# Optimization experiments

Hardware: AMD Instinct MI355X
Metric: run time of the kernel (lower is better)

Reference implementation:

```python
import jax, jax.numpy as jnp
import numpy as np

DIM0, DIMO, WIDTH, DEPTH = 64, 16, 128, 6  # depth = number of weight matrices
N = 524288


def setup_inputs() -> dict:
    key = jax.random.key(0)
    ks = jax.random.split(key, DEPTH + 1)
    x = jax.random.normal(ks[0], (N, DIM0), dtype=jnp.float32)
    bd0 = 1.0 / np.sqrt(DIM0)   # first layer init bound (per torch code)
    bd = 1.0 / np.sqrt(WIDTH)   # remaining layers init bound
    W0 = jax.random.uniform(ks[1], (DIM0, WIDTH), minval=-bd0, maxval=bd0, dtype=jnp.float32)
    W1 = jax.random.uniform(ks[2], (WIDTH, WIDTH), minval=-bd, maxval=bd, dtype=jnp.float32)
    W2 = jax.random.uniform(ks[3], (WIDTH, WIDTH), minval=-bd, maxval=bd, dtype=jnp.float32)
    W3 = jax.random.uniform(ks[4], (WIDTH, WIDTH), minval=-bd, maxval=bd, dtype=jnp.float32)
    W4 = jax.random.uniform(ks[5], (WIDTH, WIDTH), minval=-bd, maxval=bd, dtype=jnp.float32)
    W5 = jax.random.uniform(ks[6], (WIDTH, DIMO), minval=-bd, maxval=bd, dtype=jnp.float32)
    bias = jnp.zeros((DIMO,), dtype=jnp.float32)
    return {"x": x, "W0": W0, "W1": W1, "W2": W2, "W3": W3, "W4": W4, "W5": W5, "bias": bias}


def reference(x, W0, W1, W2, W3, W4, W5, bias):
    # Fully-fused MLP math: matmul (no bias) + ReLU for every layer except the
    # last (output_activation='None'); then cast back to x dtype and add bias.
    h = jax.nn.relu(x @ W0)
    h = jax.nn.relu(h @ W1)
    h = jax.nn.relu(h @ W2)
    h = jax.nn.relu(h @ W3)
    h = jax.nn.relu(h @ W4)
    out = (h @ W5).astype(x.dtype) + bias
    return out
```

## Files before the change

kernel.cpp:

```cpp
#include <hip/hip_runtime.h>
#include <stdint.h>


typedef __bf16 bf16x8 __attribute__((ext_vector_type(8)));
typedef float  floatx4 __attribute__((ext_vector_type(4)));

#define GAS __attribute__((address_space(1)))
#define LAS __attribute__((address_space(3)))

constexpr int NS   = 524288;
constexpr int SPW  = 64;
constexpr int NBLK = NS / (8 * SPW);

constexpr int WTOT = 9472;

__device__ __host__ __forceinline__ int kappa(int s) {
  return 32 * (s >> 5) + 16 * ((s >> 2) & 1) + 4 * ((s >> 3) & 3) + (s & 3);
}

__global__ void prep_weights(const float* __restrict__ W0, const float* __restrict__ W1,
                             const float* __restrict__ W2, const float* __restrict__ W3,
                             const float* __restrict__ W4, const float* __restrict__ W5,
                             bf16x8* __restrict__ ws) {
  int gid = blockIdx.x * blockDim.x + threadIdx.x;
  if (gid >= WTOT) return;
  const float* Wsrc; int nout, kt_n, base, ident;
  if (gid < 1024)      { Wsrc = W0; nout = 128; kt_n = 2; base = 0;    ident = 1; }
  else if (gid < 3072) { Wsrc = W1; nout = 128; kt_n = 4; base = 1024; ident = 0; }
  else if (gid < 5120) { Wsrc = W2; nout = 128; kt_n = 4; base = 3072; ident = 0; }
  else if (gid < 7168) { Wsrc = W3; nout = 128; kt_n = 4; base = 5120; ident = 0; }
  else if (gid < 9216) { Wsrc = W4; nout = 128; kt_n = 4; base = 7168; ident = 0; }
  else                 { Wsrc = W5; nout = 16;  kt_n = 4; base = 9216; ident = 0; }
  int id   = gid - base;
  int lane = id & 63;
  int frag = id >> 6;
  int kt   = frag % kt_n;
  int rb   = frag / kt_n;
  int outf = rb * 16 + (lane & 15);
  int gg   = lane >> 4;
  bf16x8 v;
#pragma unroll
  for (int e = 0; e < 8; ++e) {
    int s  = 32 * kt + 8 * gg + e;
    int in = ident ? s : kappa(s);
    v[e] = (__bf16)Wsrc[in * nout + outf];
  }
  ws[gid] = v;
}

__device__ __forceinline__ void pack_relu(const floatx4 acc[8][4], bf16x8 B[4][4]) {
#pragma unroll
  for (int kt = 0; kt < 4; ++kt)
#pragma unroll
    for (int i = 0; i < 4; ++i) {
      floatx4 u = acc[2 * kt][i], v = acc[2 * kt + 1][i];
      bf16x8 b;
      b[0] = (__bf16)fmaxf(u[0], 0.f); b[1] = (__bf16)fmaxf(u[1], 0.f);
      b[2] = (__bf16)fmaxf(u[2], 0.f); b[3] = (__bf16)fmaxf(u[3], 0.f);
      b[4] = (__bf16)fmaxf(v[0], 0.f); b[5] = (__bf16)fmaxf(v[1], 0.f);
      b[6] = (__bf16)fmaxf(v[2], 0.f); b[7] = (__bf16)fmaxf(v[3], 0.f);
      B[kt][i] = b;
    }
}

#define SB __builtin_amdgcn_sched_barrier(0)
#define LDH(buf, fb, fs) do {                      \
    buf[0] = Wlds[(fb) * 64 + lane];               \
    buf[1] = Wlds[((fb) + (fs)) * 64 + lane];      \
    buf[2] = Wlds[((fb) + 2 * (fs)) * 64 + lane];  \
    buf[3] = Wlds[((fb) + 3 * (fs)) * 64 + lane];  \
  } while (0)
#define MMZ(buf, kt, oh) do {                                                             \
    _Pragma("unroll") for (int j = 0; j < 4; ++j) {                                       \
      _Pragma("unroll") for (int i = 0; i < 4; ++i)                                       \
        acc[(oh) * 4 + j][i] =                                                            \
            __builtin_amdgcn_mfma_f32_16x16x32_bf16(buf[j], B[kt][i], z, 0, 0, 0);        \
    }                                                                                     \
  } while (0)
#define MMA(buf, kt, oh) do {                                                             \
    _Pragma("unroll") for (int j = 0; j < 4; ++j) {                                       \
      _Pragma("unroll") for (int i = 0; i < 4; ++i)                                       \
        acc[(oh) * 4 + j][i] = __builtin_amdgcn_mfma_f32_16x16x32_bf16(                   \
            buf[j], B[kt][i], acc[(oh) * 4 + j][i], 0, 0, 0);                             \
    }                                                                                     \
  } while (0)
#define HLAYER(Fb, NB, NS_) do {                   \
    LDH(A1, (Fb) + 16, 4); MMZ(A0, 0, 0); SB;      \
    LDH(A0, (Fb) + 1,  4); MMZ(A1, 0, 1); SB;      \
    LDH(A1, (Fb) + 17, 4); MMA(A0, 1, 0); SB;      \
    LDH(A0, (Fb) + 2,  4); MMA(A1, 1, 1); SB;      \
    LDH(A1, (Fb) + 18, 4); MMA(A0, 2, 0); SB;      \
    LDH(A0, (Fb) + 3,  4); MMA(A1, 2, 1); SB;      \
    LDH(A1, (Fb) + 19, 4); MMA(A0, 3, 0); SB;      \
    LDH(A0, (NB), (NS_)); MMA(A1, 3, 1); SB;       \
  } while (0)

__global__ void __launch_bounds__(512, 2) mlp_kernel(const float* __restrict__ x,
                                                     const float* __restrict__ bias,
                                                     const bf16x8* __restrict__ wimg,
                                                     float* __restrict__ out) {
  __shared__ bf16x8 Wlds[WTOT];

  const int t    = threadIdx.x;
  const int lane = t & 63;
  const int l15  = lane & 15;
  const int g    = lane >> 4;
  const int w    = __builtin_amdgcn_readfirstlane(t >> 6);

#pragma unroll
  for (int r = 0; r < 19; ++r) {
    int base = r * 512 + w * 64;
    if (base < WTOT)
      __builtin_amdgcn_global_load_lds((const GAS void*)(wimg + base + lane),
                                       (LAS void*)(Wlds + base), 16, 0, 0);
  }
  __syncthreads();

  const int wid = __builtin_amdgcn_readfirstlane(blockIdx.x * 8 + w);
  const size_t sbase = (size_t)wid * SPW;

  bf16x8  B[4][4];
  floatx4 acc[8][4];
  bf16x8  A0[4], A1[4];
  floatx4 z = {0.f, 0.f, 0.f, 0.f};

  LDH(A0, 0, 2);

  const float* xw = x + sbase * 64;
#pragma unroll
  for (int kt = 0; kt < 2; ++kt)
#pragma unroll
    for (int i = 0; i < 4; ++i) {
      const floatx4* p = (const floatx4*)(xw + (16 * i + l15) * 64 + 32 * kt + 8 * g);
      floatx4 lo = p[0], hi = p[1];
      bf16x8 v;
      v[0] = (__bf16)lo[0]; v[1] = (__bf16)lo[1]; v[2] = (__bf16)lo[2]; v[3] = (__bf16)lo[3];
      v[4] = (__bf16)hi[0]; v[5] = (__bf16)hi[1]; v[6] = (__bf16)hi[2]; v[7] = (__bf16)hi[3];
      B[kt][i] = v;
    }

  LDH(A1, 8, 2);  MMZ(A0, 0, 0); SB;
  LDH(A0, 1, 2);  MMZ(A1, 0, 1); SB;
  LDH(A1, 9, 2);  MMA(A0, 1, 0); SB;
  LDH(A0, 16, 4); MMA(A1, 1, 1); SB;
  pack_relu(acc, B);

  HLAYER(16,  48, 4);  pack_relu(acc, B);
  HLAYER(48,  80, 4);  pack_relu(acc, B);
  HLAYER(80, 112, 4);  pack_relu(acc, B);
  HLAYER(112, 144, 1); pack_relu(acc, B);

  floatx4 o[4];
#pragma unroll
  for (int i = 0; i < 4; ++i)
    o[i] = __builtin_amdgcn_mfma_f32_16x16x32_bf16(A0[0], B[0][i], z, 0, 0, 0);
#pragma unroll
  for (int kt = 1; kt < 4; ++kt)
#pragma unroll
    for (int i = 0; i < 4; ++i)
      o[i] = __builtin_amdgcn_mfma_f32_16x16x32_bf16(A0[kt], B[kt][i], o[i], 0, 0, 0);

  floatx4 bv = *(const floatx4*)(bias + 4 * g);
  floatx4* outv = (floatx4*)out;
#pragma unroll
  for (int i = 0; i < 4; ++i) {
    size_t s = sbase + 16 * i + l15;
    outv[s * 4 + g] = o[i] + bv;
  }
}

extern "C" void kernel_launch(void* const* d_in, const int* in_sizes, int n_in,
                              void* d_out, int out_size, void* d_ws, size_t ws_size,
                              hipStream_t stream) {
  (void)in_sizes; (void)n_in; (void)out_size; (void)ws_size;
  const float* x    = (const float*)d_in[0];
  const float* W0   = (const float*)d_in[1];
  const float* W1   = (const float*)d_in[2];
  const float* W2   = (const float*)d_in[3];
  const float* W3   = (const float*)d_in[4];
  const float* W4   = (const float*)d_in[5];
  const float* W5   = (const float*)d_in[6];
  const float* bias = (const float*)d_in[7];
  bf16x8* ws = (bf16x8*)d_ws;

  prep_weights<<<(WTOT + 255) / 256, 256, 0, stream>>>(W0, W1, W2, W3, W4, W5, ws);
  mlp_kernel<<<NBLK, 512, 0, stream>>>(x, bias, (const bf16x8*)ws, (float*)d_out);
}
```

Before: 261.7 us.

## Hand-schedule LDS weight reads with inline asm and explicit lgkmcnt waits

Replaces compiler-generated LDS fragment loads with inline-asm ds_read_b128 using immediate offsets from three base addresses. The weight reads run in a four-buffer rotation with explicit s_waitcnt lgkmcnt(4), so each MFMA group starts as soon as its own operands arrive while the next reads stay in flight. The aim is to cut address arithmetic and overly conservative waits between LDS reads and MFMAs. Inline asm hides these dependencies from the compiler, so correctness relies on the manual waitcnt counting being right, including around the global x loads.

```diff
diff --git a/kernel.cpp b/kernel.cpp
--- a/kernel.cpp
+++ b/kernel.cpp
@@ -48,6 +48,10 @@
   ws[gid] = v;
 }
 
+__device__ __forceinline__ bf16x8 asb(floatx4 v) {
+  union { floatx4 f; bf16x8 b; } u; u.f = v; return u.b;
+}
+
 __device__ __forceinline__ void pack_relu(const floatx4 acc[8][4], bf16x8 B[4][4]) {
 #pragma unroll
   for (int kt = 0; kt < 4; ++kt)
@@ -64,35 +68,35 @@
 }
 
 #define SB __builtin_amdgcn_sched_barrier(0)
-#define LDH(buf, fb, fs) do {                      \
-    buf[0] = Wlds[(fb) * 64 + lane];               \
-    buf[1] = Wlds[((fb) + (fs)) * 64 + lane];      \
-    buf[2] = Wlds[((fb) + 2 * (fs)) * 64 + lane];  \
-    buf[3] = Wlds[((fb) + 3 * (fs)) * 64 + lane];  \
-  } while (0)
-#define MMZ(buf, kt, oh) do {                                                             \
-    _Pragma("unroll") for (int j = 0; j < 4; ++j) {                                       \
-      _Pragma("unroll") for (int i = 0; i < 4; ++i)                                       \
-        acc[(oh) * 4 + j][i] =                                                            \
-            __builtin_amdgcn_mfma_f32_16x16x32_bf16(buf[j], B[kt][i], z, 0, 0, 0);        \
-    }                                                                                     \
-  } while (0)
-#define MMA(buf, kt, oh) do {                                                             \
-    _Pragma("unroll") for (int j = 0; j < 4; ++j) {                                       \
-      _Pragma("unroll") for (int i = 0; i < 4; ++i)                                       \
-        acc[(oh) * 4 + j][i] = __builtin_amdgcn_mfma_f32_16x16x32_bf16(                   \
-            buf[j], B[kt][i], acc[(oh) * 4 + j][i], 0, 0, 0);                             \
-    }                                                                                     \
-  } while (0)
-#define HLAYER(Fb, NB, NS_) do {                   \
-    LDH(A1, (Fb) + 16, 4); MMZ(A0, 0, 0); SB;      \
-    LDH(A0, (Fb) + 1,  4); MMZ(A1, 0, 1); SB;      \
-    LDH(A1, (Fb) + 17, 4); MMA(A0, 1, 0); SB;      \
-    LDH(A0, (Fb) + 2,  4); MMA(A1, 1, 1); SB;      \
-    LDH(A1, (Fb) + 18, 4); MMA(A0, 2, 0); SB;      \
-    LDH(A0, (Fb) + 3,  4); MMA(A1, 2, 1); SB;      \
-    LDH(A1, (Fb) + 19, 4); MMA(A0, 3, 0); SB;      \
-    LDH(A0, (NB), (NS_)); MMA(A1, 3, 1); SB;       \
+#define DSR(dst, f) asm volatile("ds_read_b128 %0, %1 offset:%c2"                      \
+    : "=v"(dst) : "v"((f) < 64 ? a0 : (f) < 128 ? a1 : a2), "i"((((f) & 63) * 1024)))
+#define WAITK(n) asm volatile("s_waitcnt lgkmcnt(" #n ")")
+#define MM4Z(buf, kt, j) do { _Pragma("unroll") for (int i = 0; i < 4; ++i)            \
+    acc[j][i] = __builtin_amdgcn_mfma_f32_16x16x32_bf16(asb(buf), B[kt][i], z, 0, 0, 0); } while (0)
+#define MM4A(buf, kt, j) do { _Pragma("unroll") for (int i = 0; i < 4; ++i)            \
+    acc[j][i] = __builtin_amdgcn_mfma_f32_16x16x32_bf16(asb(buf), B[kt][i], acc[j][i], 0, 0, 0); } while (0)
+#define STZ(bm, bl, f1, f2, kt, j0) \
+  DSR(bl##a, f1); DSR(bl##b, f2); WAITK(4); SB; MM4Z(bm##a, kt, j0); MM4Z(bm##b, kt, (j0) + 1)
+#define STA(bm, bl, f1, f2, kt, j0) \
+  DSR(bl##a, f1); DSR(bl##b, f2); WAITK(4); SB; MM4A(bm##a, kt, j0); MM4A(bm##b, kt, (j0) + 1)
+
+#define HLAYER(F, T1a, T1b, T2a, T2b) do {        \
+    STZ(b0, b2, (F)+16, (F)+20, 0, 0);            \
+    STZ(b1, b3, (F)+24, (F)+28, 0, 2);            \
+    STZ(b2, b0, (F)+1,  (F)+5,  0, 4);            \
+    STZ(b3, b1, (F)+9,  (F)+13, 0, 6);            \
+    STA(b0, b2, (F)+17, (F)+21, 1, 0);            \
+    STA(b1, b3, (F)+25, (F)+29, 1, 2);            \
+    STA(b2, b0, (F)+2,  (F)+6,  1, 4);            \
+    STA(b3, b1, (F)+10, (F)+14, 1, 6);            \
+    STA(b0, b2, (F)+18, (F)+22, 2, 0);            \
+    STA(b1, b3, (F)+26, (F)+30, 2, 2);            \
+    STA(b2, b0, (F)+3,  (F)+7,  2, 4);            \
+    STA(b3, b1, (F)+11, (F)+15, 2, 6);            \
+    STA(b0, b2, (F)+19, (F)+23, 3, 0);            \
+    STA(b1, b3, (F)+27, (F)+31, 3, 2);            \
+    STA(b2, b0, (T1a),  (T1b),  3, 4);            \
+    STA(b3, b1, (T2a),  (T2b),  3, 6);            \
   } while (0)
 
 __global__ void __launch_bounds__(512, 2) mlp_kernel(const float* __restrict__ x,
@@ -116,22 +120,24 @@
   }
   __syncthreads();
 
+  const uint32_t a0 = (uint32_t)(uintptr_t)((LAS void*)Wlds) + (uint32_t)lane * 16u;
+  const uint32_t a1 = a0 + 65536u;
+  const uint32_t a2 = a0 + 131072u;
+
   const int wid = __builtin_amdgcn_readfirstlane(blockIdx.x * 8 + w);
   const size_t sbase = (size_t)wid * SPW;
 
   bf16x8  B[4][4];
   floatx4 acc[8][4];
-  bf16x8  A0[4], A1[4];
-  floatx4 z = {0.f, 0.f, 0.f, 0.f};
-
-  LDH(A0, 0, 2);
-
-  const float* xw = x + sbase * 64;
+  floatx4 b0a, b0b, b1a, b1b, b2a, b2b, b3a, b3b;
+  const floatx4 z = {0.f, 0.f, 0.f, 0.f};
+
+  const GAS float* xw = (const GAS float*)x + sbase * 64;
 #pragma unroll
   for (int kt = 0; kt < 2; ++kt)
 #pragma unroll
     for (int i = 0; i < 4; ++i) {
-      const floatx4* p = (const floatx4*)(xw + (16 * i + l15) * 64 + 32 * kt + 8 * g);
+      const GAS floatx4* p = (const GAS floatx4*)(xw + (16 * i + l15) * 64 + 32 * kt + 8 * g);
       floatx4 lo = p[0], hi = p[1];
       bf16x8 v;
       v[0] = (__bf16)lo[0]; v[1] = (__bf16)lo[1]; v[2] = (__bf16)lo[2]; v[3] = (__bf16)lo[3];
@@ -139,26 +145,39 @@
       B[kt][i] = v;
     }
 
-  LDH(A1, 8, 2);  MMZ(A0, 0, 0); SB;
-  LDH(A0, 1, 2);  MMZ(A1, 0, 1); SB;
-  LDH(A1, 9, 2);  MMA(A0, 1, 0); SB;
-  LDH(A0, 16, 4); MMA(A1, 1, 1); SB;
+  DSR(b0a, 0); DSR(b0b, 2);
+  DSR(b1a, 4); DSR(b1b, 6);
+
+  STZ(b0, b2, 8, 10, 0, 0);
+  STZ(b1, b3, 12, 14, 0, 2);
+  STZ(b2, b0, 1, 3, 0, 4);
+  STZ(b3, b1, 5, 7, 0, 6);
+  STA(b0, b2, 9, 11, 1, 0);
+  STA(b1, b3, 13, 15, 1, 2);
+  STA(b2, b0, 16, 20, 1, 4);
+  STA(b3, b1, 24, 28, 1, 6);
   pack_relu(acc, B);
 
-  HLAYER(16,  48, 4);  pack_relu(acc, B);
-  HLAYER(48,  80, 4);  pack_relu(acc, B);
-  HLAYER(80, 112, 4);  pack_relu(acc, B);
-  HLAYER(112, 144, 1); pack_relu(acc, B);
+  HLAYER(16,  48, 52, 56, 60);   pack_relu(acc, B);
+  HLAYER(48,  80, 84, 88, 92);   pack_relu(acc, B);
+  HLAYER(80, 112, 116, 120, 124); pack_relu(acc, B);
+  HLAYER(112, 144, 145, 146, 147); pack_relu(acc, B);
 
   floatx4 o[4];
-#pragma unroll
-  for (int i = 0; i < 4; ++i)
-    o[i] = __builtin_amdgcn_mfma_f32_16x16x32_bf16(A0[0], B[0][i], z, 0, 0, 0);
-#pragma unroll
-  for (int kt = 1; kt < 4; ++kt)
-#pragma unroll
-    for (int i = 0; i < 4; ++i)
-      o[i] = __builtin_amdgcn_mfma_f32_16x16x32_bf16(A0[kt], B[kt][i], o[i], 0, 0, 0);
+  WAITK(2); SB;
+#pragma unroll
+  for (int i = 0; i < 4; ++i)
+    o[i] = __builtin_amdgcn_mfma_f32_16x16x32_bf16(asb(b0a), B[0][i], z, 0, 0, 0);
+#pragma unroll
+  for (int i = 0; i < 4; ++i)
+    o[i] = __builtin_amdgcn_mfma_f32_16x16x32_bf16(asb(b0b), B[1][i], o[i], 0, 0, 0);
+  WAITK(0); SB;
+#pragma unroll
+  for (int i = 0; i < 4; ++i)
+    o[i] = __builtin_amdgcn_mfma_f32_16x16x32_bf16(asb(b1a), B[2][i], o[i], 0, 0, 0);
+#pragma unroll
+  for (int i = 0; i < 4; ++i)
+    o[i] = __builtin_amdgcn_mfma_f32_16x16x32_bf16(asb(b1b), B[3][i], o[i], 0, 0, 0);
 
   floatx4 bv = *(const floatx4*)(bias + 4 * g);
   floatx4* outv = (floatx4*)out;
```

After: 251.6 us. 3.9% less time.
